# Performance work log

Measured on AMD Instinct MI355X. Metric: run time of the kernel, lower is better.

The kernel has to match this reference:

```python
import jax, jax.numpy as jnp
import numpy as np

NUM_HEADS = 12
HEAD_DIM = 128
HIDDEN = 1536
SCALE = HEAD_DIM ** -0.5


def apply_rope(x, rope):
    # x: [B,H,S,D], rope: [S,1,D] -> freqs [S,D]
    freqs = rope[:, 0, :]
    cos = jnp.repeat(freqs[:, 0::2], 2, axis=-1)[None, None]  # [1,1,S,D]
    sin = jnp.repeat(freqs[:, 1::2], 2, axis=-1)[None, None]
    xr = x.reshape(*x.shape[:-1], -1, 2)
    x_real, x_imag = xr[..., 0], xr[..., 1]
    x_rot = jnp.stack([-x_imag, x_real], axis=-1).reshape(x.shape)
    return x * cos + x_rot * sin


def qkv_split(x, W):
    # x: [B,S,hidden], W: [3*H*D, hidden] (torch Linear layout)
    B, S, _ = x.shape
    y = (x @ W.T).reshape(B, S, 3, NUM_HEADS, HEAD_DIM).transpose(2, 0, 3, 1, 4)
    return y[0], y[1], y[2]  # each [B,H,S,D]


def sdpa(q, k, v):
    s = jnp.einsum('bhqd,bhkd->bhqk', q, k) * SCALE
    p = jax.nn.softmax(s, axis=-1)
    return jnp.einsum('bhqk,bhkd->bhqd', p, v)


def setup_inputs() -> dict:
    key = jax.random.key(0)
    ks = jax.random.split(key, 7)
    B, L, N = 1, 512, 4096
    txt = jax.random.normal(ks[0], (B, L, HIDDEN), dtype=jnp.float32)
    img = jax.random.normal(ks[1], (B, N, HIDDEN), dtype=jnp.float32)
    rope = jax.random.uniform(ks[2], (N, 1, HEAD_DIM), dtype=jnp.float32)
    s = 0.02
    W_txt_qkv = jax.random.normal(ks[3], (3 * NUM_HEADS * HEAD_DIM, HIDDEN), dtype=jnp.float32) * s
    W_img_qkv = jax.random.normal(ks[4], (3 * NUM_HEADS * HEAD_DIM, HIDDEN), dtype=jnp.float32) * s
    W_txt_out = jax.random.normal(ks[5], (HIDDEN, NUM_HEADS * HEAD_DIM), dtype=jnp.float32) * s
    W_img_out = jax.random.normal(ks[6], (HIDDEN, NUM_HEADS * HEAD_DIM), dtype=jnp.float32) * s
    return {'txt': txt, 'img': img, 'rope': rope, 'W_txt_qkv': W_txt_qkv,
            'W_img_qkv': W_img_qkv, 'W_txt_out': W_txt_out, 'W_img_out': W_img_out}


def reference(txt, img, rope, W_txt_qkv, W_img_qkv, W_txt_out, W_img_out):
    B, L, _ = txt.shape
    _, N, _ = img.shape
    txt_q, txt_k, txt_v = qkv_split(txt, W_txt_qkv)
    img_q, img_k, img_v = qkv_split(img, W_img_qkv)
    img_q = apply_rope(img_q, rope)
    img_k = apply_rope(img_k, rope)
    k = jnp.concatenate([txt_k, img_k], axis=2)  # [B,H,L+N,D]
    v = jnp.concatenate([txt_v, img_v], axis=2)
    txt_o = sdpa(txt_q, k, v).transpose(0, 2, 1, 3).reshape(B, L, -1)
    img_o = sdpa(img_q, k, v).transpose(0, 2, 1, 3).reshape(B, N, -1)
    return txt_o @ W_txt_out.T, img_o @ W_img_out.T
```

## Files before the change

kernel.cpp:

```cpp
#include <hip/hip_runtime.h>
#include <hip/hip_bf16.h>
#include <stdint.h>


typedef __attribute__((ext_vector_type(8)))  short bf16x8;
typedef __attribute__((ext_vector_type(4)))  float f32x4;
typedef __attribute__((ext_vector_type(16))) float f32x16;
typedef __attribute__((ext_vector_type(4)))  short s16x4;

#define NUM_HEADS 12
#define HEAD_DIM  128
#define HIDDEN    1536
#define LTXT      512
#define NIMG      4096
#define STOT      4608
#define QKV3      4608
#define SCALE_Q2  (0.08838834764831845f * 1.44269504088896340f)
#define DEFER_THR 12.0f

__device__ __forceinline__ float b2f(short s) {
    union { uint32_t u; float f; } c; c.u = ((uint32_t)(uint16_t)s) << 16; return c.f;
}
__device__ __forceinline__ short f2b(float f) {
    union { float f; uint32_t u; } c; c.f = f;
    uint32_t u = c.u + 0x7FFFu + ((c.u >> 16) & 1u);
    return (short)(u >> 16);
}
__device__ __forceinline__ float fexp2(float x) {
#if __has_builtin(__builtin_amdgcn_exp2f)
    return __builtin_amdgcn_exp2f(x);
#else
    return exp2f(x);
#endif
}
__device__ __forceinline__ uint32_t cvt_pk_bf16(float lo, float hi) {
    uint32_t r;
    asm("v_cvt_pk_bf16_f32 %0, %1, %2" : "=v"(r) : "v"(lo), "v"(hi));
    return r;
}
__device__ __forceinline__ void permlane32_swap(uint32_t& a, uint32_t& b) {
    asm("v_permlane32_swap_b32 %0, %1" : "+v"(a), "+v"(b));
}

typedef const void __attribute__((address_space(1)))* gas_p;
typedef void __attribute__((address_space(3)))* las_p;
__device__ __forceinline__ void gload_lds16(const void* g, void* l) {
    __builtin_amdgcn_global_load_lds((gas_p)g, (las_p)l, 16, 0, 0);
}

__global__ __launch_bounds__(256) void cast6(
    const float* __restrict__ s0, const float* __restrict__ s1,
    const float* __restrict__ s2, const float* __restrict__ s3,
    const float* __restrict__ s4, const float* __restrict__ s5,
    short* __restrict__ dst)
{
    size_t i = (size_t)blockIdx.x * 256 + threadIdx.x;
    const size_t e0 = 98304, e1 = 884736, e2 = 1769472,
                 e3 = 2654208, e4 = 2949120;
    const float* src; size_t base;
    if (i < e2) {
        if (i < e0)      { src = s0; base = 0;  }
        else if (i < e1) { src = s1; base = e0; }
        else             { src = s2; base = e1; }
    } else {
        if (i < e3)      { src = s3; base = e2; }
        else if (i < e4) { src = s4; base = e3; }
        else             { src = s5; base = e4; }
    }
    const float4* p = (const float4*)src + (i - base) * 2;
    float4 a = p[0], b = p[1];
    bf16x8 o;
    o[0] = f2b(a.x); o[1] = f2b(a.y); o[2] = f2b(a.z); o[3] = f2b(a.w);
    o[4] = f2b(b.x); o[5] = f2b(b.y); o[6] = f2b(b.z); o[7] = f2b(b.w);
    *((bf16x8*)dst + i) = o;
}

template <typename OT>
__global__ __launch_bounds__(256) void gemm_bt2(
    const short* __restrict__ A, const short* __restrict__ B0,
    const short* __restrict__ B1, OT* __restrict__ C,
    int M, int N, int K, int rowsplit)
{
    __shared__ __align__(16) short As[2][128 * 32];
    __shared__ __align__(16) short Bs[2][128 * 32];
    const int t    = threadIdx.x;
    const int lane = t & 63, wid = t >> 6;
    const int wr = wid >> 1, wc = wid & 1;
    const int l15 = lane & 15, lk = lane >> 4;
    const int bm = blockIdx.y, bn = blockIdx.x;

    const short* B = (bm * 128 < rowsplit) ? B0 : B1;
    const int srow = t >> 2, skg = t & 3;
    const short* Ag = A + (size_t)(bm * 128 + srow) * K + skg * 8;
    const short* Bg = B + (size_t)(bn * 128 + srow) * K + skg * 8;
    const size_t rowblk = (size_t)64 * K;

    f32x4 acc[4][4];
    const f32x4 z = {0.f, 0.f, 0.f, 0.f};
#pragma unroll
    for (int i = 0; i < 4; ++i)
#pragma unroll
        for (int j = 0; j < 4; ++j) acc[i][j] = z;

    auto STAGE = [&](int b, int kt) {
        const int k0 = kt * 32;
        gload_lds16(Ag + k0,          &As[b][wid * 512]);
        gload_lds16(Ag + rowblk + k0, &As[b][2048 + wid * 512]);
        gload_lds16(Bg + k0,          &Bs[b][wid * 512]);
        gload_lds16(Bg + rowblk + k0, &Bs[b][2048 + wid * 512]);
    };

    const int NT = K / 32;
    STAGE(0, 0);
    for (int kt = 0; kt < NT; ++kt) {
        const int cur = kt & 1;
        if (kt + 1 < NT) {
            STAGE(cur ^ 1, kt + 1);
            asm volatile("s_waitcnt vmcnt(4)" ::: "memory");
        } else {
            asm volatile("s_waitcnt vmcnt(0)" ::: "memory");
        }
        __builtin_amdgcn_s_barrier();

        bf16x8 af[4], bfr[4];
#pragma unroll
        for (int i = 0; i < 4; ++i)
            af[i] = *(const bf16x8*)&As[cur][(wr * 64 + i * 16 + l15) * 32 + lk * 8];
#pragma unroll
        for (int j = 0; j < 4; ++j)
            bfr[j] = *(const bf16x8*)&Bs[cur][(wc * 64 + j * 16 + l15) * 32 + lk * 8];
        __builtin_amdgcn_s_setprio(1);
#pragma unroll
        for (int i = 0; i < 4; ++i)
#pragma unroll
            for (int j = 0; j < 4; ++j)
                acc[i][j] = __builtin_amdgcn_mfma_f32_16x16x32_bf16(
                    af[i], bfr[j], acc[i][j], 0, 0, 0);
        __builtin_amdgcn_s_setprio(0);

        asm volatile("s_waitcnt lgkmcnt(0)" ::: "memory");
        __builtin_amdgcn_sched_barrier(0);
        __builtin_amdgcn_s_barrier();
    }

#pragma unroll
    for (int i = 0; i < 4; ++i) {
#pragma unroll
        for (int j = 0; j < 4; ++j) {
            const int row0 = bm * 128 + wr * 64 + i * 16 + lk * 4;
            const int col  = bn * 128 + wc * 64 + j * 16 + l15;
#pragma unroll
            for (int r = 0; r < 4; ++r) {
                float v = acc[i][j][r];
                if constexpr (sizeof(OT) == 2)
                    C[(size_t)(row0 + r) * N + col] = (OT)f2b(v);
                else
                    C[(size_t)(row0 + r) * N + col] = v;
            }
        }
    }
}

__global__ __launch_bounds__(256) void pack_qkv(
    const short* __restrict__ Y, const float* __restrict__ rope,
    short* __restrict__ Qb, short* __restrict__ Kb, short* __restrict__ VTb)
{
    const int st = blockIdx.x, h = blockIdx.y, t = threadIdx.x;
    const int s0 = st * 64;
    __shared__ __align__(16) short Vt[128][72];

#pragma unroll
    for (int i = 0; i < 4; ++i) {
        int e  = t + i * 256;
        int sl = e >> 4, dg = e & 15;
        int s  = s0 + sl;
        const short* src = Y + (size_t)s * QKV3;
        bf16x8 q8 = *(const bf16x8*)(src + h * 128 + dg * 8);
        bf16x8 k8 = *(const bf16x8*)(src + (12 + h) * 128 + dg * 8);
        bf16x8 v8 = *(const bf16x8*)(src + (24 + h) * 128 + dg * 8);
        float qf[8], kf[8];
#pragma unroll
        for (int j = 0; j < 8; ++j) { qf[j] = b2f(q8[j]); kf[j] = b2f(k8[j]); }
        if (s >= LTXT) {
            const float* rp = rope + (size_t)(s - LTXT) * 128 + dg * 8;
            float4 r0 = *(const float4*)rp;
            float4 r1 = *(const float4*)(rp + 4);
            float rr[8] = {r0.x, r0.y, r0.z, r0.w, r1.x, r1.y, r1.z, r1.w};
#pragma unroll
            for (int j = 0; j < 4; ++j) {
                float c = rr[2 * j], sn = rr[2 * j + 1];
                float q0 = qf[2 * j], q1 = qf[2 * j + 1];
                qf[2 * j] = q0 * c - q1 * sn; qf[2 * j + 1] = q1 * c + q0 * sn;
                float k0 = kf[2 * j], k1 = kf[2 * j + 1];
                kf[2 * j] = k0 * c - k1 * sn; kf[2 * j + 1] = k1 * c + k0 * sn;
            }
        }
        bf16x8 qo, ko;
#pragma unroll
        for (int j = 0; j < 8; ++j) { qo[j] = f2b(qf[j] * SCALE_Q2); ko[j] = f2b(kf[j]); }
        *(bf16x8*)(Qb + ((size_t)h * STOT + s) * 128 + dg * 8) = qo;
        *(bf16x8*)(Kb + ((size_t)h * STOT + s) * 128 + dg * 8) = ko;
#pragma unroll
        for (int j = 0; j < 8; ++j) Vt[dg * 8 + j][sl] = v8[j];
    }
    __syncthreads();
#pragma unroll
    for (int i = 0; i < 4; ++i) {
        int c = t + i * 256;
        int d = c >> 3, sg = c & 7;
        bf16x8 val = *(const bf16x8*)&Vt[d][sg * 8];
        *(bf16x8*)(VTb + ((size_t)h * 128 + d) * STOT + s0 + sg * 8) = val;
    }
}

__global__ __launch_bounds__(512, 2) void attn_fwd(
    const short* __restrict__ Q, const short* __restrict__ Kb,
    const short* __restrict__ VT, short* __restrict__ O)
{
    const int id  = blockIdx.x;
    const int swz = (id & 7) * 27 + (id >> 3);
    const int qb  = swz % 18, h = swz / 18;

    const int t = threadIdx.x;
    const int lane = t & 63, wid = t >> 6;
    const int l31 = lane & 31, hi = lane >> 5;
    const int xorb = l31 & 7;

    __shared__ __align__(16) short KV[4][2][64 * 128];

    const short* Qrow = Q + ((size_t)h * STOT + qb * 256 + wid * 32 + l31) * 128;
    bf16x8 qf[8];
#pragma unroll
    for (int dk = 0; dk < 8; ++dk)
        qf[dk] = *(const bf16x8*)(Qrow + dk * 16 + hi * 8);

    f32x16 o[4];
#pragma unroll
    for (int nt = 0; nt < 4; ++nt)
#pragma unroll
        for (int r = 0; r < 16; ++r) o[nt][r] = 0.f;
    float m = -1e30f, den = 0.f;

    const short* Kh = Kb + (size_t)h * STOT * 128;
    const short* Vh = VT + (size_t)h * 128 * STOT;

    const short* Ksrc[2]; const short* Vsrc[2];
#pragma unroll
    for (int i = 0; i < 2; ++i) {
        int p = t + i * 512;
        int krow = p >> 4, kx = (p & 15) ^ (krow & 7);
        Ksrc[i] = Kh + (size_t)krow * 128 + kx * 8;
        int vrow = p >> 3, vx = (p & 7) ^ (vrow & 7);
        Vsrc[i] = Vh + (size_t)vrow * STOT + vx * 8;
    }

    auto STAGE = [&](int b, int kb) {
#pragma unroll
        for (int i = 0; i < 2; ++i) {
            gload_lds16(Ksrc[i] + (size_t)kb * 8192, &KV[b][0][i * 4096 + wid * 512]);
            gload_lds16(Vsrc[i] + (size_t)kb * 64,   &KV[b][1][i * 4096 + wid * 512]);
        }
    };

    int kaddr[8], vaddr[4];
#pragma unroll
    for (int dk = 0; dk < 8; ++dk)
        kaddr[dk] = l31 * 256 + (((dk * 2 + hi) ^ xorb) << 4);
#pragma unroll
    for (int s = 0; s < 4; ++s)
        vaddr[s] = l31 * 128 + (((s * 2 + hi) ^ xorb) << 4);

    const char* Kb4[4] = { (const char*)&KV[0][0][0], (const char*)&KV[1][0][0],
                           (const char*)&KV[2][0][0], (const char*)&KV[3][0][0] };
    const char* Vb4[4] = { (const char*)&KV[0][1][0], (const char*)&KV[1][1][0],
                           (const char*)&KV[2][1][0], (const char*)&KV[3][1][0] };

    auto QK = [&](const char* Ksc, f32x16& s0, f32x16& s1) {
#pragma unroll
        for (int r = 0; r < 16; ++r) { s0[r] = 0.f; s1[r] = 0.f; }
        __builtin_amdgcn_s_setprio(1);
#pragma unroll
        for (int dk = 0; dk < 8; ++dk) {
            bf16x8 kf0 = *(const bf16x8*)(Ksc + kaddr[dk]);
            bf16x8 kf1 = *(const bf16x8*)(Ksc + kaddr[dk] + 8192);
            s0 = __builtin_amdgcn_mfma_f32_32x32x16_bf16(kf0, qf[dk], s0, 0, 0, 0);
            s1 = __builtin_amdgcn_mfma_f32_32x32x16_bf16(kf1, qf[dk], s1, 0, 0, 0);
        }
        __builtin_amdgcn_s_setprio(0);
    };

    auto SMPV = [&](const char* Vsc, f32x16& s0, f32x16& s1) {
        float v = s0[0];
#pragma unroll
        for (int r = 1; r < 16; ++r) v = fmaxf(v, s0[r]);
#pragma unroll
        for (int r = 0; r < 16; ++r) v = fmaxf(v, s1[r]);
        v = fmaxf(v, __shfl_xor(v, 32));
        if (__any(v > m + DEFER_THR)) {
            float mn = fmaxf(m, v);
            float al = fexp2(m - mn);
            m = mn;
            den *= al;
#pragma unroll
            for (int nt = 0; nt < 4; ++nt)
#pragma unroll
                for (int r = 0; r < 16; ++r) o[nt][r] *= al;
        }
        float rs = 0.f;
#pragma unroll
        for (int r = 0; r < 16; ++r) { s0[r] = fexp2(s0[r] - m); rs += s0[r]; }
#pragma unroll
        for (int r = 0; r < 16; ++r) { s1[r] = fexp2(s1[r] - m); rs += s1[r]; }
        rs += __shfl_xor(rs, 32);
        den += rs;

        __builtin_amdgcn_s_setprio(1);
#pragma unroll
        for (int s = 0; s < 4; ++s) {
            const f32x16& pe = (s < 2) ? s0 : s1;
            const int rb = (s & 1) * 8;
            uint32_t a0 = cvt_pk_bf16(pe[rb + 0], pe[rb + 1]);
            uint32_t a1 = cvt_pk_bf16(pe[rb + 2], pe[rb + 3]);
            uint32_t a2 = cvt_pk_bf16(pe[rb + 4], pe[rb + 5]);
            uint32_t a3 = cvt_pk_bf16(pe[rb + 6], pe[rb + 7]);
            permlane32_swap(a0, a2);
            permlane32_swap(a1, a3);
            union { uint32_t u[4]; bf16x8 v8; } pb;
            pb.u[0] = a0; pb.u[1] = a1; pb.u[2] = a2; pb.u[3] = a3;
#pragma unroll
            for (int nt = 0; nt < 4; ++nt) {
                bf16x8 vf = *(const bf16x8*)(Vsc + vaddr[s] + nt * 4096);
                o[nt] = __builtin_amdgcn_mfma_f32_32x32x16_bf16(vf, pb.v8, o[nt], 0, 0, 0);
            }
        }
        __builtin_amdgcn_s_setprio(0);
    };

    f32x16 scA0, scA1, scB0, scB1;

    STAGE(0, 0);
    STAGE(1, 1);
    asm volatile("s_waitcnt vmcnt(4)" ::: "memory");
    __builtin_amdgcn_s_barrier();
    QK(Kb4[0], scA0, scA1);

    for (int jb = 0; jb < 68; jb += 4) {
        STAGE(2, jb + 2);
        asm volatile("s_waitcnt vmcnt(4)" ::: "memory");
        __builtin_amdgcn_s_barrier();
        QK(Kb4[1], scB0, scB1);
        SMPV(Vb4[0], scA0, scA1);

        STAGE(3, jb + 3);
        asm volatile("s_waitcnt vmcnt(4)" ::: "memory");
        __builtin_amdgcn_s_barrier();
        QK(Kb4[2], scA0, scA1);
        SMPV(Vb4[1], scB0, scB1);

        STAGE(0, jb + 4);
        asm volatile("s_waitcnt vmcnt(4)" ::: "memory");
        __builtin_amdgcn_s_barrier();
        QK(Kb4[3], scB0, scB1);
        SMPV(Vb4[2], scA0, scA1);

        STAGE(1, jb + 5);
        asm volatile("s_waitcnt vmcnt(4)" ::: "memory");
        __builtin_amdgcn_s_barrier();
        QK(Kb4[0], scA0, scA1);
        SMPV(Vb4[3], scB0, scB1);
    }
    STAGE(2, 70);
    asm volatile("s_waitcnt vmcnt(4)" ::: "memory");
    __builtin_amdgcn_s_barrier();
    QK(Kb4[1], scB0, scB1);
    SMPV(Vb4[0], scA0, scA1);

    STAGE(3, 71);
    asm volatile("s_waitcnt vmcnt(4)" ::: "memory");
    __builtin_amdgcn_s_barrier();
    QK(Kb4[2], scA0, scA1);
    SMPV(Vb4[1], scB0, scB1);

    asm volatile("s_waitcnt vmcnt(0)" ::: "memory");
    __builtin_amdgcn_s_barrier();
    QK(Kb4[3], scB0, scB1);
    SMPV(Vb4[2], scA0, scA1);

    SMPV(Vb4[3], scB0, scB1);

    const int qrow = qb * 256 + wid * 32 + l31;
    float inv = 1.0f / den;
    short* Orow = O + (size_t)qrow * HIDDEN + h * 128;
#pragma unroll
    for (int nt = 0; nt < 4; ++nt) {
#pragma unroll
        for (int g = 0; g < 4; ++g) {
            s16x4 w4;
#pragma unroll
            for (int j = 0; j < 4; ++j) w4[j] = f2b(o[nt][g * 4 + j] * inv);
            *(s16x4*)(Orow + nt * 32 + g * 8 + hi * 4) = w4;
        }
    }
}

extern "C" void kernel_launch(void* const* d_in, const int* in_sizes, int n_in,
                              void* d_out, int out_size, void* d_ws, size_t ws_size,
                              hipStream_t stream)
{
    (void)in_sizes; (void)n_in; (void)out_size; (void)ws_size;
    const float* txt  = (const float*)d_in[0];
    const float* img  = (const float*)d_in[1];
    const float* rope = (const float*)d_in[2];
    const float* Wtq  = (const float*)d_in[3];
    const float* Wiq  = (const float*)d_in[4];
    const float* Wto  = (const float*)d_in[5];
    const float* Wio  = (const float*)d_in[6];
    float* out = (float*)d_out;

    short* w = (short*)d_ws;
    size_t off = 0;
    auto alloc = [&](size_t elems) { short* p = w + off; off += elems; return p; };
    short* txtb = alloc((size_t)LTXT * HIDDEN);
    short* imgb = alloc((size_t)NIMG * HIDDEN);
    short* Wtqb = alloc((size_t)QKV3 * HIDDEN);
    short* Wiqb = alloc((size_t)QKV3 * HIDDEN);
    short* Wtob = alloc((size_t)HIDDEN * HIDDEN);
    short* Wiob = alloc((size_t)HIDDEN * HIDDEN);
    short* Yt   = alloc((size_t)LTXT * QKV3);
    short* Yi   = alloc((size_t)NIMG * QKV3);
    short* Qb   = alloc((size_t)NUM_HEADS * STOT * HEAD_DIM);
    short* Kb   = alloc((size_t)NUM_HEADS * STOT * HEAD_DIM);
    short* VTb  = alloc((size_t)NUM_HEADS * STOT * HEAD_DIM);
    (void)imgb; (void)Yi;
    short* Ob   = txtb;

    cast6<<<12672, 256, 0, stream>>>(txt, img, Wtq, Wiq, Wto, Wio, txtb);

    gemm_bt2<short><<<dim3(QKV3 / 128, STOT / 128), 256, 0, stream>>>(
        txtb, Wtqb, Wiqb, Yt, STOT, QKV3, HIDDEN, LTXT);

    pack_qkv<<<dim3(STOT / 64, NUM_HEADS), 256, 0, stream>>>(
        Yt, rope, Qb, Kb, VTb);

    attn_fwd<<<dim3(STOT / 256 * NUM_HEADS), 512, 0, stream>>>(Qb, Kb, VTb, Ob);

    gemm_bt2<float><<<dim3(HIDDEN / 128, STOT / 128), 256, 0, stream>>>(
        Ob, Wtob, Wiob, out, STOT, HIDDEN, HIDDEN, LTXT);
}
```

Before: 301.5 us.

## Add 256x256-tile QKV GEMM with async LDS loads and phased MFMA schedule

Replaces the 128x128 QKV projection GEMM with a new 512-thread kernel using 256x256 output tiles, K-step 64, swizzled direct global-to-LDS loads, double buffering, and a four-phase MFMA schedule with setprio hints. Larger tiles raise arithmetic intensity and cut global traffic per FLOP. The grid shrinks to 18x18 blocks, which may underfill the CUs, and the large accumulator footprint risks register pressure. The kernel hardcodes 24 K iterations, which only holds for K=1536.

```diff
diff --git a/kernel.cpp b/kernel.cpp
--- a/kernel.cpp
+++ b/kernel.cpp
@@ -75,6 +75,161 @@
     *((bf16x8*)dst + i) = o;
 }
 
+__global__ __launch_bounds__(512, 2) void gemm256(
+    const short* __restrict__ A, const short* __restrict__ B0,
+    const short* __restrict__ B1, short* __restrict__ C,
+    int M, int N, int K, int rowsplit)
+{
+    __shared__ __align__(16) short GL[2][2][256 * 64];
+    const int t = threadIdx.x;
+    const int lane = t & 63, wid = t >> 6;
+    const int wr = wid >> 2, wc = wid & 3;
+    const int l15 = lane & 15, lk = lane >> 4;
+    const int bm = blockIdx.y, bn = blockIdx.x;
+
+    const short* B = (bm * 256 < rowsplit) ? B0 : B1;
+
+    const short* Asrc[4]; const short* Bsrc[4];
+#pragma unroll
+    for (int i = 0; i < 4; ++i) {
+        int p = t + i * 512;
+        int row = p >> 3, glog = (p & 7) ^ (row & 7);
+        Asrc[i] = A + (size_t)(bm * 256 + row) * K + glog * 8;
+        Bsrc[i] = B + (size_t)(bn * 256 + row) * K + glog * 8;
+    }
+
+    auto STAGE = [&](int b, int j) {
+        const int k0 = j * 64;
+#pragma unroll
+        for (int i = 0; i < 4; ++i) {
+            gload_lds16(Asrc[i] + k0, &GL[b][0][(i * 512 + wid * 64) * 8]);
+            gload_lds16(Bsrc[i] + k0, &GL[b][1][(i * 512 + wid * 64) * 8]);
+        }
+    };
+
+    int abase[2], bbase[2];
+#pragma unroll
+    for (int s2 = 0; s2 < 2; ++s2) {
+        int x = ((s2 * 4 + lk) ^ (l15 & 7)) << 4;
+        abase[s2] = (wr * 128 + l15) * 128 + x;
+        bbase[s2] = (wc * 64 + l15) * 128 + x;
+    }
+
+    f32x4 acc[8][4];
+    const f32x4 z = {0.f, 0.f, 0.f, 0.f};
+#pragma unroll
+    for (int i = 0; i < 8; ++i)
+#pragma unroll
+        for (int j = 0; j < 4; ++j) acc[i][j] = z;
+
+    auto PHASES = [&](int b) {
+        const char* Ab = (const char*)&GL[b][0][0];
+        const char* Bb = (const char*)&GL[b][1][0];
+        bf16x8 af[4][2], bq0[2][2], bq1[2][2];
+
+#pragma unroll
+        for (int mf = 0; mf < 4; ++mf)
+#pragma unroll
+            for (int s2 = 0; s2 < 2; ++s2)
+                af[mf][s2] = *(const bf16x8*)(Ab + abase[s2] + mf * 2048);
+#pragma unroll
+        for (int nf = 0; nf < 2; ++nf)
+#pragma unroll
+            for (int s2 = 0; s2 < 2; ++s2)
+                bq0[nf][s2] = *(const bf16x8*)(Bb + bbase[s2] + nf * 2048);
+        __builtin_amdgcn_s_setprio(1);
+#pragma unroll
+        for (int mf = 0; mf < 4; ++mf)
+#pragma unroll
+            for (int nf = 0; nf < 2; ++nf)
+#pragma unroll
+                for (int s2 = 0; s2 < 2; ++s2)
+                    acc[mf][nf] = __builtin_amdgcn_mfma_f32_16x16x32_bf16(
+                        af[mf][s2], bq0[nf][s2], acc[mf][nf], 0, 0, 0);
+        __builtin_amdgcn_s_setprio(0);
+        __builtin_amdgcn_s_barrier();
+
+#pragma unroll
+        for (int nf = 0; nf < 2; ++nf)
+#pragma unroll
+            for (int s2 = 0; s2 < 2; ++s2)
+                bq1[nf][s2] = *(const bf16x8*)(Bb + bbase[s2] + (nf + 2) * 2048);
+        __builtin_amdgcn_s_setprio(1);
+#pragma unroll
+        for (int mf = 0; mf < 4; ++mf)
+#pragma unroll
+            for (int nf = 0; nf < 2; ++nf)
+#pragma unroll
+                for (int s2 = 0; s2 < 2; ++s2)
+                    acc[mf][nf + 2] = __builtin_amdgcn_mfma_f32_16x16x32_bf16(
+                        af[mf][s2], bq1[nf][s2], acc[mf][nf + 2], 0, 0, 0);
+        __builtin_amdgcn_s_setprio(0);
+        __builtin_amdgcn_s_barrier();
+
+#pragma unroll
+        for (int mf = 0; mf < 4; ++mf)
+#pragma unroll
+            for (int s2 = 0; s2 < 2; ++s2)
+                af[mf][s2] = *(const bf16x8*)(Ab + abase[s2] + (mf + 4) * 2048);
+        __builtin_amdgcn_s_setprio(1);
+#pragma unroll
+        for (int mf = 0; mf < 4; ++mf)
+#pragma unroll
+            for (int nf = 0; nf < 2; ++nf)
+#pragma unroll
+                for (int s2 = 0; s2 < 2; ++s2)
+                    acc[mf + 4][nf] = __builtin_amdgcn_mfma_f32_16x16x32_bf16(
+                        af[mf][s2], bq0[nf][s2], acc[mf + 4][nf], 0, 0, 0);
+        __builtin_amdgcn_s_setprio(0);
+        __builtin_amdgcn_s_barrier();
+
+        __builtin_amdgcn_s_setprio(1);
+#pragma unroll
+        for (int mf = 0; mf < 4; ++mf)
+#pragma unroll
+            for (int nf = 0; nf < 2; ++nf)
+#pragma unroll
+                for (int s2 = 0; s2 < 2; ++s2)
+                    acc[mf + 4][nf + 2] = __builtin_amdgcn_mfma_f32_16x16x32_bf16(
+                        af[mf][s2], bq1[nf][s2], acc[mf + 4][nf + 2], 0, 0, 0);
+        __builtin_amdgcn_s_setprio(0);
+        asm volatile("s_waitcnt lgkmcnt(0)" ::: "memory");
+        __builtin_amdgcn_sched_barrier(0);
+        __builtin_amdgcn_s_barrier();
+    };
+
+    STAGE(0, 0);
+    for (int jj = 0; jj < 22; jj += 2) {
+        STAGE(1, jj + 1);
+        asm volatile("s_waitcnt vmcnt(8)" ::: "memory");
+        __builtin_amdgcn_s_barrier();
+        PHASES(0);
+        STAGE(0, jj + 2);
+        asm volatile("s_waitcnt vmcnt(8)" ::: "memory");
+        __builtin_amdgcn_s_barrier();
+        PHASES(1);
+    }
+    STAGE(1, 23);
+    asm volatile("s_waitcnt vmcnt(8)" ::: "memory");
+    __builtin_amdgcn_s_barrier();
+    PHASES(0);
+    asm volatile("s_waitcnt vmcnt(0)" ::: "memory");
+    __builtin_amdgcn_s_barrier();
+    PHASES(1);
+
+#pragma unroll
+    for (int mf = 0; mf < 8; ++mf) {
+#pragma unroll
+        for (int nf = 0; nf < 4; ++nf) {
+            const int row0 = bm * 256 + wr * 128 + mf * 16 + lk * 4;
+            const int col  = bn * 256 + wc * 64 + nf * 16 + l15;
+#pragma unroll
+            for (int r = 0; r < 4; ++r)
+                C[(size_t)(row0 + r) * N + col] = f2b(acc[mf][nf][r]);
+        }
+    }
+}
+
 template <typename OT>
 __global__ __launch_bounds__(256) void gemm_bt2(
     const short* __restrict__ A, const short* __restrict__ B0,
@@ -436,7 +591,7 @@
 
     cast6<<<12672, 256, 0, stream>>>(txt, img, Wtq, Wiq, Wto, Wio, txtb);
 
-    gemm_bt2<short><<<dim3(QKV3 / 128, STOT / 128), 256, 0, stream>>>(
+    gemm256<<<dim3(QKV3 / 256, STOT / 256), 512, 0, stream>>>(
         txtb, Wtqb, Wiqb, Yt, STOT, QKV3, HIDDEN, LTXT);
 
     pack_qkv<<<dim3(STOT / 64, NUM_HEADS), 256, 0, stream>>>(
```

Result: slower. 309.1 us (+2.5%).

## Fuse RoPE and QKV packing into projection GEMM epilogues, compute V transposed

Applied to the files above, without the earlier changes.

Replaces the QKV projection GEMM plus separate pack kernel with two GEMMs. One writes Q and K directly in head-major layout, applying RoPE via lane shuffles and scaling Q in its epilogue. The other computes V^T directly by swapping operands. This removes the intermediate Y buffer round trip and the pack/transpose kernel. The epilogue stores are scalar bf16 with per-element rope loads, which may be less efficient than vectorized writes.

```diff
diff --git a/kernel.cpp b/kernel.cpp
--- a/kernel.cpp
+++ b/kernel.cpp
@@ -75,6 +75,185 @@
     *((bf16x8*)dst + i) = o;
 }
 
+__global__ __launch_bounds__(256) void gemm_qk(
+    const short* __restrict__ A, const short* __restrict__ B0,
+    const short* __restrict__ B1, const float* __restrict__ rope,
+    short* __restrict__ Qb, short* __restrict__ Kb, int K)
+{
+    __shared__ __align__(16) short As[2][128 * 32];
+    __shared__ __align__(16) short Bs[2][128 * 32];
+    const int t    = threadIdx.x;
+    const int lane = t & 63, wid = t >> 6;
+    const int wr = wid >> 1, wc = wid & 1;
+    const int l15 = lane & 15, lk = lane >> 4;
+    const int bm = blockIdx.y, bn = blockIdx.x;
+
+    const short* B = (bm < 4) ? B0 : B1;
+    const int srow = t >> 2, skg = t & 3;
+    const short* Ag = A + (size_t)(bm * 128 + srow) * K + skg * 8;
+    const short* Bg = B + (size_t)(bn * 128 + srow) * K + skg * 8;
+    const size_t rowblk = (size_t)64 * K;
+
+    f32x4 acc[4][4];
+    const f32x4 z = {0.f, 0.f, 0.f, 0.f};
+#pragma unroll
+    for (int i = 0; i < 4; ++i)
+#pragma unroll
+        for (int j = 0; j < 4; ++j) acc[i][j] = z;
+
+    auto STAGE = [&](int b, int kt) {
+        const int k0 = kt * 32;
+        gload_lds16(Ag + k0,          &As[b][wid * 512]);
+        gload_lds16(Ag + rowblk + k0, &As[b][2048 + wid * 512]);
+        gload_lds16(Bg + k0,          &Bs[b][wid * 512]);
+        gload_lds16(Bg + rowblk + k0, &Bs[b][2048 + wid * 512]);
+    };
+
+    const int NT = K / 32;
+    STAGE(0, 0);
+    for (int kt = 0; kt < NT; ++kt) {
+        const int cur = kt & 1;
+        if (kt + 1 < NT) {
+            STAGE(cur ^ 1, kt + 1);
+            asm volatile("s_waitcnt vmcnt(4)" ::: "memory");
+        } else {
+            asm volatile("s_waitcnt vmcnt(0)" ::: "memory");
+        }
+        __builtin_amdgcn_s_barrier();
+
+        bf16x8 af[4], bfr[4];
+#pragma unroll
+        for (int i = 0; i < 4; ++i)
+            af[i] = *(const bf16x8*)&As[cur][(wr * 64 + i * 16 + l15) * 32 + lk * 8];
+#pragma unroll
+        for (int j = 0; j < 4; ++j)
+            bfr[j] = *(const bf16x8*)&Bs[cur][(wc * 64 + j * 16 + l15) * 32 + lk * 8];
+        __builtin_amdgcn_s_setprio(1);
+#pragma unroll
+        for (int i = 0; i < 4; ++i)
+#pragma unroll
+            for (int j = 0; j < 4; ++j)
+                acc[i][j] = __builtin_amdgcn_mfma_f32_16x16x32_bf16(
+                    af[i], bfr[j], acc[i][j], 0, 0, 0);
+        __builtin_amdgcn_s_setprio(0);
+
+        asm volatile("s_waitcnt lgkmcnt(0)" ::: "memory");
+        __builtin_amdgcn_sched_barrier(0);
+        __builtin_amdgcn_s_barrier();
+    }
+
+    const bool isQ = (bn < 12);
+    const int h = isQ ? bn : bn - 12;
+    short* Out = isQ ? Qb : Kb;
+    const bool doRope = (bm >= 4);
+#pragma unroll
+    for (int i = 0; i < 4; ++i) {
+#pragma unroll
+        for (int j = 0; j < 4; ++j) {
+            const int s0r = bm * 128 + wr * 64 + i * 16 + lk * 4;
+            const int d   = wc * 64 + j * 16 + l15;
+#pragma unroll
+            for (int r = 0; r < 4; ++r) {
+                float v = acc[i][j][r];
+                const int s = s0r + r;
+                if (doRope) {
+                    const float* rp = rope + (size_t)(s - LTXT) * 128 + (d & ~1);
+                    float2 cs = *(const float2*)rp;
+                    float partner = __shfl_xor(v, 1);
+                    v = v * cs.x + ((d & 1) ? partner * cs.y : -partner * cs.y);
+                }
+                if (isQ) v *= SCALE_Q2;
+                Out[((size_t)h * STOT + s) * 128 + d] = f2b(v);
+            }
+        }
+    }
+}
+
+__global__ __launch_bounds__(256) void gemm_vt(
+    const short* __restrict__ Wtv, const short* __restrict__ Wiv,
+    const short* __restrict__ Xt, const short* __restrict__ Xi,
+    short* __restrict__ VT, int K)
+{
+    __shared__ __align__(16) short As[2][128 * 32];
+    __shared__ __align__(16) short Bs[2][128 * 32];
+    const int t    = threadIdx.x;
+    const int lane = t & 63, wid = t >> 6;
+    const int wr = wid >> 1, wc = wid & 1;
+    const int l15 = lane & 15, lk = lane >> 4;
+    const int bm = blockIdx.y, bn = blockIdx.x;
+
+    const bool isTxt = (bn < 4);
+    const short* A = isTxt ? Wtv : Wiv;
+    const short* B = isTxt ? Xt : Xi;
+    const int bcol = isTxt ? bn : bn - 4;
+    const int colbase = isTxt ? 0 : LTXT;
+
+    const int srow = t >> 2, skg = t & 3;
+    const short* Ag = A + (size_t)(bm * 128 + srow) * K + skg * 8;
+    const short* Bg = B + (size_t)(bcol * 128 + srow) * K + skg * 8;
+    const size_t rowblk = (size_t)64 * K;
+
+    f32x4 acc[4][4];
+    const f32x4 z = {0.f, 0.f, 0.f, 0.f};
+#pragma unroll
+    for (int i = 0; i < 4; ++i)
+#pragma unroll
+        for (int j = 0; j < 4; ++j) acc[i][j] = z;
+
+    auto STAGE = [&](int b, int kt) {
+        const int k0 = kt * 32;
+        gload_lds16(Ag + k0,          &As[b][wid * 512]);
+        gload_lds16(Ag + rowblk + k0, &As[b][2048 + wid * 512]);
+        gload_lds16(Bg + k0,          &Bs[b][wid * 512]);
+        gload_lds16(Bg + rowblk + k0, &Bs[b][2048 + wid * 512]);
+    };
+
+    const int NT = K / 32;
+    STAGE(0, 0);
+    for (int kt = 0; kt < NT; ++kt) {
+        const int cur = kt & 1;
+        if (kt + 1 < NT) {
+            STAGE(cur ^ 1, kt + 1);
+            asm volatile("s_waitcnt vmcnt(4)" ::: "memory");
+        } else {
+            asm volatile("s_waitcnt vmcnt(0)" ::: "memory");
+        }
+        __builtin_amdgcn_s_barrier();
+
+        bf16x8 af[4], bfr[4];
+#pragma unroll
+        for (int i = 0; i < 4; ++i)
+            af[i] = *(const bf16x8*)&As[cur][(wr * 64 + i * 16 + l15) * 32 + lk * 8];
+#pragma unroll
+        for (int j = 0; j < 4; ++j)
+            bfr[j] = *(const bf16x8*)&Bs[cur][(wc * 64 + j * 16 + l15) * 32 + lk * 8];
+        __builtin_amdgcn_s_setprio(1);
+#pragma unroll
+        for (int i = 0; i < 4; ++i)
+#pragma unroll
+            for (int j = 0; j < 4; ++j)
+                acc[i][j] = __builtin_amdgcn_mfma_f32_16x16x32_bf16(
+                    af[i], bfr[j], acc[i][j], 0, 0, 0);
+        __builtin_amdgcn_s_setprio(0);
+
+        asm volatile("s_waitcnt lgkmcnt(0)" ::: "memory");
+        __builtin_amdgcn_sched_barrier(0);
+        __builtin_amdgcn_s_barrier();
+    }
+
+#pragma unroll
+    for (int i = 0; i < 4; ++i) {
+#pragma unroll
+        for (int j = 0; j < 4; ++j) {
+            const int row0 = bm * 128 + wr * 64 + i * 16 + lk * 4;
+            const int col  = colbase + bcol * 128 + wc * 64 + j * 16 + l15;
+#pragma unroll
+            for (int r = 0; r < 4; ++r)
+                VT[(size_t)(row0 + r) * STOT + col] = f2b(acc[i][j][r]);
+        }
+    }
+}
+
 template <typename OT>
 __global__ __launch_bounds__(256) void gemm_bt2(
     const short* __restrict__ A, const short* __restrict__ B0,
@@ -161,58 +340,6 @@
     }
 }
 
-__global__ __launch_bounds__(256) void pack_qkv(
-    const short* __restrict__ Y, const float* __restrict__ rope,
-    short* __restrict__ Qb, short* __restrict__ Kb, short* __restrict__ VTb)
-{
-    const int st = blockIdx.x, h = blockIdx.y, t = threadIdx.x;
-    const int s0 = st * 64;
-    __shared__ __align__(16) short Vt[128][72];
-
-#pragma unroll
-    for (int i = 0; i < 4; ++i) {
-        int e  = t + i * 256;
-        int sl = e >> 4, dg = e & 15;
-        int s  = s0 + sl;
-        const short* src = Y + (size_t)s * QKV3;
-        bf16x8 q8 = *(const bf16x8*)(src + h * 128 + dg * 8);
-        bf16x8 k8 = *(const bf16x8*)(src + (12 + h) * 128 + dg * 8);
-        bf16x8 v8 = *(const bf16x8*)(src + (24 + h) * 128 + dg * 8);
-        float qf[8], kf[8];
-#pragma unroll
-        for (int j = 0; j < 8; ++j) { qf[j] = b2f(q8[j]); kf[j] = b2f(k8[j]); }
-        if (s >= LTXT) {
-            const float* rp = rope + (size_t)(s - LTXT) * 128 + dg * 8;
-            float4 r0 = *(const float4*)rp;
-            float4 r1 = *(const float4*)(rp + 4);
-            float rr[8] = {r0.x, r0.y, r0.z, r0.w, r1.x, r1.y, r1.z, r1.w};
-#pragma unroll
-            for (int j = 0; j < 4; ++j) {
-                float c = rr[2 * j], sn = rr[2 * j + 1];
-                float q0 = qf[2 * j], q1 = qf[2 * j + 1];
-                qf[2 * j] = q0 * c - q1 * sn; qf[2 * j + 1] = q1 * c + q0 * sn;
-                float k0 = kf[2 * j], k1 = kf[2 * j + 1];
-                kf[2 * j] = k0 * c - k1 * sn; kf[2 * j + 1] = k1 * c + k0 * sn;
-            }
-        }
-        bf16x8 qo, ko;
-#pragma unroll
-        for (int j = 0; j < 8; ++j) { qo[j] = f2b(qf[j] * SCALE_Q2); ko[j] = f2b(kf[j]); }
-        *(bf16x8*)(Qb + ((size_t)h * STOT + s) * 128 + dg * 8) = qo;
-        *(bf16x8*)(Kb + ((size_t)h * STOT + s) * 128 + dg * 8) = ko;
-#pragma unroll
-        for (int j = 0; j < 8; ++j) Vt[dg * 8 + j][sl] = v8[j];
-    }
-    __syncthreads();
-#pragma unroll
-    for (int i = 0; i < 4; ++i) {
-        int c = t + i * 256;
-        int d = c >> 3, sg = c & 7;
-        bf16x8 val = *(const bf16x8*)&Vt[d][sg * 8];
-        *(bf16x8*)(VTb + ((size_t)h * 128 + d) * STOT + s0 + sg * 8) = val;
-    }
-}
-
 __global__ __launch_bounds__(512, 2) void attn_fwd(
     const short* __restrict__ Q, const short* __restrict__ Kb,
     const short* __restrict__ VT, short* __restrict__ O)
@@ -426,21 +553,19 @@
     short* Wiqb = alloc((size_t)QKV3 * HIDDEN);
     short* Wtob = alloc((size_t)HIDDEN * HIDDEN);
     short* Wiob = alloc((size_t)HIDDEN * HIDDEN);
-    short* Yt   = alloc((size_t)LTXT * QKV3);
-    short* Yi   = alloc((size_t)NIMG * QKV3);
     short* Qb   = alloc((size_t)NUM_HEADS * STOT * HEAD_DIM);
     short* Kb   = alloc((size_t)NUM_HEADS * STOT * HEAD_DIM);
     short* VTb  = alloc((size_t)NUM_HEADS * STOT * HEAD_DIM);
-    (void)imgb; (void)Yi;
     short* Ob   = txtb;
 
     cast6<<<12672, 256, 0, stream>>>(txt, img, Wtq, Wiq, Wto, Wio, txtb);
 
-    gemm_bt2<short><<<dim3(QKV3 / 128, STOT / 128), 256, 0, stream>>>(
-        txtb, Wtqb, Wiqb, Yt, STOT, QKV3, HIDDEN, LTXT);
-
-    pack_qkv<<<dim3(STOT / 64, NUM_HEADS), 256, 0, stream>>>(
-        Yt, rope, Qb, Kb, VTb);
+    gemm_qk<<<dim3(24, 36), 256, 0, stream>>>(
+        txtb, Wtqb, Wiqb, rope, Qb, Kb, HIDDEN);
+
+    gemm_vt<<<dim3(36, 12), 256, 0, stream>>>(
+        Wtqb + (size_t)3072 * HIDDEN, Wiqb + (size_t)3072 * HIDDEN,
+        txtb, imgb, VTb, HIDDEN);
 
     attn_fwd<<<dim3(STOT / 256 * NUM_HEADS), 512, 0, stream>>>(Qb, Kb, VTb, Ob);
 
```

Result: slower. 333.4 us (+10.6%).
